# Optimization experiments

Measured on AMD Instinct MI355X. Metric: run time of the kernel, lower is better.

## Reference

```python
import jax, jax.numpy as jnp
import numpy as np

B, S, E = 2, 2048, 2048
H, HKV, D = 32, 8, 64  # n_heads, n_kv_heads, head_dim


def _rope(x, cos, sin):
    # x: [B,S,h,D]; cos/sin: [1,S,1,D//2]. Complex rotate on (even,odd) pairs.
    xp = x.reshape(*x.shape[:-1], D // 2, 2)
    x0, x1 = xp[..., 0], xp[..., 1]
    r0 = x0 * cos - x1 * sin
    r1 = x0 * sin + x1 * cos
    return jnp.stack([r0, r1], axis=-1).reshape(x.shape)


def setup_inputs() -> dict:
    key = jax.random.key(0)
    ks = jax.random.split(key, 8)
    sc = 0.02
    # real RoPE frequencies (theta=10000) for realism
    inv = 1.0 / (10000.0 ** (np.arange(0, D, 2, dtype=np.float32) / D))
    t = np.arange(S, dtype=np.float32)
    ang = np.outer(t, inv)  # [S, D/2]
    return {
        "x": jax.random.normal(ks[0], (B, S, E), jnp.float32),
        "start_pos": 0,
        "freqs_cos": jnp.asarray(np.cos(ang))[None, :, None, :],
        "freqs_sin": jnp.asarray(np.sin(ang))[None, :, None, :],
        "wq": jax.random.normal(ks[1], (E, H * D), jnp.float32) * sc,
        "wk": jax.random.normal(ks[2], (E, HKV * D), jnp.float32) * sc,
        "wv": jax.random.normal(ks[3], (E, HKV * D), jnp.float32) * sc,
        "out_w": jax.random.normal(ks[4], (H * D, E), jnp.float32) * sc,
        "out_b": jnp.zeros((E,), jnp.float32),
        "k_cache": jnp.zeros((B, S, HKV, D), jnp.float32),
        "v_cache": jnp.zeros((B, S, HKV, D), jnp.float32),
    }


def reference(x, start_pos, freqs_cos, freqs_sin, wq, wk, wv, out_w, out_b, k_cache, v_cache):
    b, s, _ = x.shape
    q = (x @ wq).reshape(b, s, H, D)
    k = (x @ wk).reshape(b, s, HKV, D)
    v = (x @ wv).reshape(b, s, HKV, D)
    q = _rope(q, freqs_cos[:, :s], freqs_sin[:, :s])
    k = _rope(k, freqs_cos[:, :s], freqs_sin[:, :s])
    # KV-cache append (torch code detaches before writing)
    k_cache = jax.lax.dynamic_update_slice(k_cache, jax.lax.stop_gradient(k), (0, start_pos, 0, 0))
    v_cache = jax.lax.dynamic_update_slice(v_cache, jax.lax.stop_gradient(v), (0, start_pos, 0, 0))
    keys = k_cache[:b, : start_pos + s]    # [b, T, HKV, D]
    values = v_cache[:b, : start_pos + s]
    g = H // HKV
    if g > 1:  # GQA head repeat
        keys = jnp.repeat(keys, g, axis=2)     # [b, T, H, D]
        values = jnp.repeat(values, g, axis=2)
    scores = jnp.einsum("bqhd,bkhd->bhqk", q, keys) / jnp.sqrt(jnp.float32(D))
    att = jax.nn.softmax(scores, axis=-1)  # NOTE: source applies no causal mask
    o = jnp.einsum("bhqk,bkhd->bqhd", att, values).reshape(b, s, H * D)
    return o @ out_w + out_b
```

## Files before the change

kernel.cpp:

```cpp
#include <hip/hip_runtime.h>
#include <math.h>

#define B_    2
#define S_    2048
#define E_    2048
#define H_    32
#define HKV_  8
#define D_    64

typedef __bf16 bf16x8 __attribute__((ext_vector_type(8)));
typedef float  f32x4  __attribute__((ext_vector_type(4)));
typedef float  f32x16 __attribute__((ext_vector_type(16)));
typedef unsigned int u32x2 __attribute__((ext_vector_type(2)));
typedef unsigned int u32x4 __attribute__((ext_vector_type(4)));

#define GPTR(x) ((const __attribute__((address_space(1))) void*)(x))
#define LPTR(x) ((__attribute__((address_space(3))) void*)(x))

#define QK_SCALE_LOG2E 0.18033688011112042f

__global__ __launch_bounds__(256) void convert_kernel(
    const float* __restrict__ in, __bf16* __restrict__ out, int n8)
{
    const int i = blockIdx.x * 256 + threadIdx.x;
    if (i >= n8) return;
    const float4 a = ((const float4*)in)[i * 2];
    const float4 b = ((const float4*)in)[i * 2 + 1];
    bf16x8 o;
    o[0] = (__bf16)a.x; o[1] = (__bf16)a.y; o[2] = (__bf16)a.z; o[3] = (__bf16)a.w;
    o[4] = (__bf16)b.x; o[5] = (__bf16)b.y; o[6] = (__bf16)b.z; o[7] = (__bf16)b.w;
    ((bf16x8*)out)[i] = o;
}

__global__ __launch_bounds__(256) void transpose_convert_all_kernel(
    const float* __restrict__ wq, const float* __restrict__ wk,
    const float* __restrict__ wv, const float* __restrict__ wo,
    __bf16* __restrict__ wT, __bf16* __restrict__ woT)
{
    const float* in; __bf16* out; int N, xb;
    const int x = blockIdx.x;
    if (x < 64)      { in = wq; out = wT;                        N = 2048; xb = x; }
    else if (x < 80) { in = wk; out = wT + (size_t)2048 * 2048;  N = 512;  xb = x - 64; }
    else if (x < 96) { in = wv; out = wT + (size_t)2560 * 2048;  N = 512;  xb = x - 80; }
    else             { in = wo; out = woT;                       N = 2048; xb = x - 96; }
    const int K = 2048;

    __shared__ float tile[32][33];
    const int k0 = blockIdx.y * 32, n0 = xb * 32;
    const int r  = threadIdx.x >> 3;
    const int c4 = (threadIdx.x & 7) * 4;
    const float4 v = *(const float4*)&in[(size_t)(k0 + r) * N + n0 + c4];
    tile[r][c4 + 0] = v.x; tile[r][c4 + 1] = v.y;
    tile[r][c4 + 2] = v.z; tile[r][c4 + 3] = v.w;
    __syncthreads();
    ushort4 o;
    __bf16 h0 = (__bf16)tile[c4 + 0][r]; o.x = __builtin_bit_cast(unsigned short, h0);
    __bf16 h1 = (__bf16)tile[c4 + 1][r]; o.y = __builtin_bit_cast(unsigned short, h1);
    __bf16 h2 = (__bf16)tile[c4 + 2][r]; o.z = __builtin_bit_cast(unsigned short, h2);
    __bf16 h3 = (__bf16)tile[c4 + 3][r]; o.w = __builtin_bit_cast(unsigned short, h3);
    *(ushort4*)&out[(size_t)(n0 + r) * K + k0 + c4] = o;
}

template<int BN> struct PG {
    static constexpr int BM     = 256;
    static constexpr int BK     = 32;
    static constexpr int ASLOT  = BM * BK;
    static constexpr int BSLOT  = BN * BK;
    static constexpr int SLOT   = ASLOT + BSLOT;
    static constexpr int BINSTR = BN / 128;
    static constexpr int L      = 2 + BINSTR;
    static constexpr int NJ     = BN / 64;
};

template<int BN>
__device__ __forceinline__ void stage_tile(
    const __bf16* __restrict__ A, const __bf16* __restrict__ Bt,
    int m0, int n0, int K, int T, __bf16* sl, int t, int wbase)
{
    using G = PG<BN>;
    const int k0   = T * G::BK;
    const int rsub = t >> 2;
    const int cp   = t & 3;
#pragma unroll
    for (int g = 0; g < 2; ++g) {
        const int row = g * 128 + rsub;
        const int cl  = cp ^ ((row >> 1) & 3);
        __builtin_amdgcn_global_load_lds(
            GPTR(A + (size_t)(m0 + row) * K + k0 + cl * 8),
            LPTR(sl + (g * 512 + wbase) * 8), 16, 0, 0);
    }
#pragma unroll
    for (int g = 0; g < G::BINSTR; ++g) {
        const int row = g * 128 + rsub;
        const int cl  = cp ^ ((row >> 1) & 3);
        __builtin_amdgcn_global_load_lds(
            GPTR(Bt + (size_t)(n0 + row) * K + k0 + cl * 8),
            LPTR(sl + G::ASLOT + (g * 512 + wbase) * 8), 16, 0, 0);
    }
}

template<int BN>
__device__ __forceinline__ void compute_tile(
    const __bf16* sl, int wrow, int wcol, int col, int quad,
    f32x4 acc[8][PG<BN>::NJ])
{
    using G = PG<BN>;
    bf16x8 af[8], bfr[G::NJ];
#pragma unroll
    for (int i = 0; i < 8; ++i) {
        const int m = wrow + i * 16 + col;
        af[i] = *(const bf16x8*)&sl[m * 32 + ((quad ^ ((m >> 1) & 3)) * 8)];
    }
#pragma unroll
    for (int j = 0; j < G::NJ; ++j) {
        const int n = wcol + j * 16 + col;
        bfr[j] = *(const bf16x8*)&sl[G::ASLOT + n * 32 + ((quad ^ ((n >> 1) & 3)) * 8)];
    }
    __builtin_amdgcn_s_setprio(1);
#pragma unroll
    for (int i = 0; i < 8; ++i)
#pragma unroll
        for (int j = 0; j < G::NJ; ++j)
            acc[i][j] = __builtin_amdgcn_mfma_f32_16x16x32_bf16(
                af[i], bfr[j], acc[i][j], 0, 0, 0);
    __builtin_amdgcn_s_setprio(0);
}

template<int BN>
__device__ __forceinline__ void gemm_pipe_body(
    const __bf16* __restrict__ A, const __bf16* __restrict__ Bt,
    int m0, int n0, int K, __bf16* sL, f32x4 acc[8][PG<BN>::NJ])
{
    using G = PG<BN>;
    const int t     = threadIdx.x;
    const int wbase = t & ~63;
    const int lane  = t & 63;
    const int col   = lane & 15;
    const int quad  = lane >> 4;
    const int w     = t >> 6;
    const int wrow  = (w >> 2) * 128;
    const int wcol  = (w & 3) * (BN / 4);
    const int NT    = K / G::BK;

    stage_tile<BN>(A, Bt, m0, n0, K, 0, sL + 0 * G::SLOT, t, wbase);
    stage_tile<BN>(A, Bt, m0, n0, K, 1, sL + 1 * G::SLOT, t, wbase);
    stage_tile<BN>(A, Bt, m0, n0, K, 2, sL + 2 * G::SLOT, t, wbase);

    int T = 0;
#pragma unroll 1
    for (; T < NT - 3; ++T) {
        asm volatile("s_waitcnt vmcnt(%0)" :: "n"(2 * G::L) : "memory");
        __builtin_amdgcn_s_barrier();
        stage_tile<BN>(A, Bt, m0, n0, K, T + 3, sL + ((T + 3) & 3) * G::SLOT, t, wbase);
        compute_tile<BN>(sL + (T & 3) * G::SLOT, wrow, wcol, col, quad, acc);
    }
    asm volatile("s_waitcnt vmcnt(%0)" :: "n"(2 * G::L) : "memory");
    __builtin_amdgcn_s_barrier();
    compute_tile<BN>(sL + (T & 3) * G::SLOT, wrow, wcol, col, quad, acc); ++T;
    asm volatile("s_waitcnt vmcnt(%0)" :: "n"(G::L) : "memory");
    __builtin_amdgcn_s_barrier();
    compute_tile<BN>(sL + (T & 3) * G::SLOT, wrow, wcol, col, quad, acc); ++T;
    asm volatile("s_waitcnt vmcnt(0)" ::: "memory");
    __builtin_amdgcn_s_barrier();
    compute_tile<BN>(sL + (T & 3) * G::SLOT, wrow, wcol, col, quad, acc);
}

__global__ __launch_bounds__(512, 2) void gemm_qkv_kernel(
    const __bf16* __restrict__ xb, const __bf16* __restrict__ wT,
    const float* __restrict__ fc, const float* __restrict__ fs,
    __bf16* __restrict__ qb, __bf16* __restrict__ kb, __bf16* __restrict__ vb)
{
    __shared__ __bf16 sL[4 * PG<256>::SLOT];
    f32x4 acc[8][4];
#pragma unroll
    for (int i = 0; i < 8; ++i)
#pragma unroll
        for (int j = 0; j < 4; ++j) acc[i][j] = (f32x4){0.f, 0.f, 0.f, 0.f};

    const int lin     = blockIdx.x;
    const int logical = (lin & 7) * 24 + (lin >> 3);
    const int bx      = logical % 12;
    const int m0      = (logical / 12) * 256;
    const int n0      = bx * 256;

    gemm_pipe_body<256>(xb, wT, m0, n0, E_, sL, acc);

    __bf16* Cp; int ldc, base;
    if (bx < 8)       { Cp = qb; ldc = H_ * D_;   base = 0;    }
    else if (bx < 10) { Cp = kb; ldc = HKV_ * D_; base = 2048; }
    else              { Cp = vb; ldc = HKV_ * D_; base = 2560; }
    const bool  doRope = (bx < 10);
    const float qsc    = (bx < 8) ? QK_SCALE_LOG2E : 1.0f;

    const int t    = threadIdx.x;
    const int lane = t & 63;
    const int col  = lane & 15;
    const int quad = lane >> 4;
    const int w    = t >> 6;
    const int wrow = (w >> 2) * 128;
    const int wcol = (w & 3) * 64;
#pragma unroll
    for (int i = 0; i < 8; ++i)
#pragma unroll
        for (int j = 0; j < 4; ++j)
#pragma unroll
            for (int r = 0; r < 4; ++r) {
                const int m  = m0 + wrow + i * 16 + quad * 4 + r;
                const int ng = n0 + wcol + j * 16 + col;
                float val = acc[i][j][r] * qsc;
                if (doRope) {
                    const int   s    = m & (S_ - 1);
                    const int   pair = (ng & 63) >> 1;
                    const float c    = fc[s * 32 + pair];
                    const float sn   = fs[s * 32 + pair];
                    const float oth  = __shfl_xor(val, 1);
                    val = (lane & 1) ? (oth * sn + val * c)
                                     : (val * c - oth * sn);
                }
                Cp[(size_t)m * ldc + (ng - base)] = (__bf16)val;
            }
}

__global__ __launch_bounds__(512, 2) void gemm_out_kernel(
    const __bf16* __restrict__ ob, const __bf16* __restrict__ woT,
    const float* __restrict__ bias, float* __restrict__ out)
{
    __shared__ __bf16 sL[4 * PG<128>::SLOT];
    f32x4 acc[8][2];
#pragma unroll
    for (int i = 0; i < 8; ++i)
#pragma unroll
        for (int j = 0; j < 2; ++j) acc[i][j] = (f32x4){0.f, 0.f, 0.f, 0.f};

    const int lin     = blockIdx.x;
    const int logical = (lin & 7) * 32 + (lin >> 3);
    const int n0      = (logical % 16) * 128;
    const int m0      = (logical / 16) * 256;

    gemm_pipe_body<128>(ob, woT, m0, n0, H_ * D_, sL, acc);

    const int t    = threadIdx.x;
    const int lane = t & 63;
    const int col  = lane & 15;
    const int quad = lane >> 4;
    const int w    = t >> 6;
    const int wrow = (w >> 2) * 128;
    const int wcol = (w & 3) * 32;
#pragma unroll
    for (int i = 0; i < 8; ++i)
#pragma unroll
        for (int j = 0; j < 2; ++j)
#pragma unroll
            for (int r = 0; r < 4; ++r) {
                const int m = m0 + wrow + i * 16 + quad * 4 + r;
                const int n = n0 + wcol + j * 16 + col;
                out[(size_t)m * E_ + n] = acc[i][j][r] + bias[n];
            }
}

struct StageRegs {
    bf16x8  k0, k1;
    ushort4 va0, vc0, va1, vc1;
};

__device__ __forceinline__ void stage_load(
    StageRegs& r, const __bf16* kbase, const __bf16* vbase, int j0,
    int kkey, int kd, int vkp, int vdg)
{
    const int KSTR = HKV_ * D_;
    const __bf16* kr = kbase + (size_t)(j0 + kkey) * KSTR + kd;
    r.k0 = ((const bf16x8*)kr)[0];
    r.k1 = ((const bf16x8*)kr)[1];
    const __bf16* v0 = vbase + (size_t)(j0 + vkp) * KSTR + vdg;
    r.va0 = *(const ushort4*)(v0);
    r.vc0 = *(const ushort4*)(v0 + KSTR);
    r.va1 = *(const ushort4*)(v0 + 32);
    r.vc1 = *(const ushort4*)(v0 + KSTR + 32);
}

__device__ __forceinline__ void stage_write(
    const StageRegs& r, __bf16 (*sK)[72], __bf16 (*sVT)[72],
    int kkey, int kd, int vkp, int vdg)
{
    *(bf16x8*)&sK[kkey][kd]     = r.k0;
    *(bf16x8*)&sK[kkey][kd + 8] = r.k1;
    *(unsigned int*)&sVT[vdg + 0][vkp]      = ((unsigned)r.vc0.x << 16) | r.va0.x;
    *(unsigned int*)&sVT[vdg + 1][vkp]      = ((unsigned)r.vc0.y << 16) | r.va0.y;
    *(unsigned int*)&sVT[vdg + 2][vkp]      = ((unsigned)r.vc0.z << 16) | r.va0.z;
    *(unsigned int*)&sVT[vdg + 3][vkp]      = ((unsigned)r.vc0.w << 16) | r.va0.w;
    *(unsigned int*)&sVT[vdg + 32 + 0][vkp] = ((unsigned)r.vc1.x << 16) | r.va1.x;
    *(unsigned int*)&sVT[vdg + 32 + 1][vkp] = ((unsigned)r.vc1.y << 16) | r.va1.y;
    *(unsigned int*)&sVT[vdg + 32 + 2][vkp] = ((unsigned)r.vc1.z << 16) | r.va1.z;
    *(unsigned int*)&sVT[vdg + 32 + 3][vkp] = ((unsigned)r.vc1.w << 16) | r.va1.w;
}

__device__ __forceinline__ bf16x8 pack_pa(const f32x16& p, int i0)
{
    unsigned a0, a1, a2, a3;
    asm("v_cvt_pk_bf16_f32 %0, %1, %2" : "=v"(a0) : "v"(p[i0 + 0]), "v"(p[i0 + 1]));
    asm("v_cvt_pk_bf16_f32 %0, %1, %2" : "=v"(a1) : "v"(p[i0 + 2]), "v"(p[i0 + 3]));
    asm("v_cvt_pk_bf16_f32 %0, %1, %2" : "=v"(a2) : "v"(p[i0 + 4]), "v"(p[i0 + 5]));
    asm("v_cvt_pk_bf16_f32 %0, %1, %2" : "=v"(a3) : "v"(p[i0 + 6]), "v"(p[i0 + 7]));
    const u32x2 s02 = __builtin_amdgcn_permlane32_swap(a0, a2, false, false);
    const u32x2 s13 = __builtin_amdgcn_permlane32_swap(a1, a3, false, false);
    return __builtin_bit_cast(bf16x8, (u32x4){s02[0], s13[0], s02[1], s13[1]});
}

__device__ __forceinline__ void attn_tile(
    const __bf16 (*sK)[72], const __bf16 (*sVT)[72],
    const bf16x8* bQ, int lq, int hi,
    f32x16& O0, f32x16& O1, float& lsum)
{
    f32x16 p0, p1;
#pragma unroll
    for (int i = 0; i < 16; ++i) { p0[i] = 0.f; p1[i] = 0.f; }
    __builtin_amdgcn_s_setprio(1);
#pragma unroll
    for (int ks = 0; ks < 4; ++ks) {
        const bf16x8 aK0 = *(const bf16x8*)&sK[lq][ks * 16 + hi * 8];
        const bf16x8 aK1 = *(const bf16x8*)&sK[32 + lq][ks * 16 + hi * 8];
        p0 = __builtin_amdgcn_mfma_f32_32x32x16_bf16(aK0, bQ[ks], p0, 0, 0, 0);
        p1 = __builtin_amdgcn_mfma_f32_32x32x16_bf16(aK1, bQ[ks], p1, 0, 0, 0);
    }
    __builtin_amdgcn_s_setprio(0);

    bf16x8 vbf[8];
#pragma unroll
    for (int ks = 0; ks < 4; ++ks) {
        vbf[ks * 2]     = *(const bf16x8*)&sVT[lq][ks * 16 + hi * 8];
        vbf[ks * 2 + 1] = *(const bf16x8*)&sVT[32 + lq][ks * 16 + hi * 8];
    }

    float ps = 0.f;
#pragma unroll
    for (int i = 0; i < 16; ++i) {
        p0[i] = __builtin_amdgcn_exp2f(p0[i]);
        p1[i] = __builtin_amdgcn_exp2f(p1[i]);
        ps += p0[i] + p1[i];
    }
    lsum += ps;

    bf16x8 pa[4];
    pa[0] = pack_pa(p0, 0);
    pa[1] = pack_pa(p0, 8);
    pa[2] = pack_pa(p1, 0);
    pa[3] = pack_pa(p1, 8);

    __builtin_amdgcn_s_setprio(1);
#pragma unroll
    for (int ks = 0; ks < 4; ++ks) {
        O0 = __builtin_amdgcn_mfma_f32_32x32x16_bf16(pa[ks], vbf[ks * 2],     O0, 0, 0, 0);
        O1 = __builtin_amdgcn_mfma_f32_32x32x16_bf16(pa[ks], vbf[ks * 2 + 1], O1, 0, 0, 0);
    }
    __builtin_amdgcn_s_setprio(0);
}

__global__ __launch_bounds__(256) void attn_kernel(
    const __bf16* __restrict__ qw, const __bf16* __restrict__ kw,
    const __bf16* __restrict__ vw, __bf16* __restrict__ ow)
{
    __shared__ __bf16 sK0[64][72], sVT0[64][72];
    __shared__ __bf16 sK1[64][72], sVT1[64][72];

    const int t    = threadIdx.x;
    const int lane = t & 63;
    const int w    = t >> 6;
    const int lq   = lane & 31;
    const int hi   = lane >> 5;

    const int bh  = blockIdx.y;
    const int b   = bh >> 5;
    const int h   = bh & 31;
    const int kvh = h >> 2;
    const int q0  = blockIdx.x * 128 + w * 32;

    bf16x8 bQ[4];
    {
        const __bf16* qrow = qw + (((size_t)b * S_ + q0 + lq) * H_ + h) * D_;
#pragma unroll
        for (int ks = 0; ks < 4; ++ks)
            bQ[ks] = *(const bf16x8*)(qrow + ks * 16 + hi * 8);
    }

    f32x16 O0, O1;
#pragma unroll
    for (int i = 0; i < 16; ++i) { O0[i] = 0.f; O1[i] = 0.f; }
    float lsum = 0.f;

    const __bf16* kbase = kw + ((size_t)b * S_ * HKV_ + kvh) * D_;
    const __bf16* vbase = vw + ((size_t)b * S_ * HKV_ + kvh) * D_;
    const int kkey = t >> 2,        kd  = (t & 3) * 16;
    const int vkp  = (t & 31) * 2,  vdg = (t >> 5) * 4;

    StageRegs sr;
    stage_load(sr, kbase, vbase, 0, kkey, kd, vkp, vdg);
    stage_write(sr, sK0, sVT0, kkey, kd, vkp, vdg);
    __syncthreads();

#pragma unroll 1
    for (int j0 = 0; j0 < S_; j0 += 128) {
        StageRegs nx;
        stage_load(nx, kbase, vbase, j0 + 64, kkey, kd, vkp, vdg);
        attn_tile(sK0, sVT0, bQ, lq, hi, O0, O1, lsum);
        stage_write(nx, sK1, sVT1, kkey, kd, vkp, vdg);
        __syncthreads();
        if (j0 + 128 < S_)
            stage_load(nx, kbase, vbase, j0 + 128, kkey, kd, vkp, vdg);
        attn_tile(sK1, sVT1, bQ, lq, hi, O0, O1, lsum);
        if (j0 + 128 < S_)
            stage_write(nx, sK0, sVT0, kkey, kd, vkp, vdg);
        __syncthreads();
    }

    lsum += __shfl_xor(lsum, 32);
    const float inv = 1.0f / lsum;

#pragma unroll
    for (int r = 0; r < 16; ++r) {
        const int   qr = (r & 3) + 8 * (r >> 2) + 4 * hi;
        const float li = __shfl(inv, qr);
        __bf16* orow = ow + (((size_t)b * S_ + q0 + qr) * H_ + h) * D_;
        orow[lq]      = (__bf16)(O0[r] * li);
        orow[32 + lq] = (__bf16)(O1[r] * li);
    }
}

extern "C" void kernel_launch(void* const* d_in, const int* in_sizes, int n_in,
                              void* d_out, int out_size, void* d_ws, size_t ws_size,
                              hipStream_t stream)
{
    const float* x  = (const float*)d_in[0];
    const float* fc = (const float*)d_in[2];
    const float* fs = (const float*)d_in[3];
    const float* wq = (const float*)d_in[4];
    const float* wk = (const float*)d_in[5];
    const float* wv = (const float*)d_in[6];
    const float* wo = (const float*)d_in[7];
    const float* obias = (const float*)d_in[8];
    float* out = (float*)d_out;

    __bf16* ws  = (__bf16*)d_ws;
    __bf16* xb  = ws;
    __bf16* wT  = xb  + (size_t)4096 * 2048;
    __bf16* woT = wT  + (size_t)3072 * 2048;
    __bf16* qb  = woT + (size_t)2048 * 2048;
    __bf16* kb  = qb  + (size_t)B_ * S_ * H_ * D_;
    __bf16* vb  = kb  + (size_t)B_ * S_ * HKV_ * D_;
    __bf16* obf = vb  + (size_t)B_ * S_ * HKV_ * D_;

    convert_kernel<<<4096, 256, 0, stream>>>(x, xb, 4096 * 2048 / 8);
    transpose_convert_all_kernel<<<dim3(160, 64), 256, 0, stream>>>(
        wq, wk, wv, wo, wT, woT);

    gemm_qkv_kernel<<<192, 512, 0, stream>>>(xb, wT, fc, fs, qb, kb, vb);

    attn_kernel<<<dim3(S_ / 128, B_ * H_), 256, 0, stream>>>(qb, kb, vb, obf);

    gemm_out_kernel<<<256, 512, 0, stream>>>(obf, woT, obias, out);
}
```

Baseline: 353.4 us.

## Process two 32-row query tiles per wave to reuse K/V shared-memory fragments

Each wave now handles 64 query rows (two 32-row sub-tiles) instead of 32. The K and V^T fragments are loaded from LDS once per 64-key tile and reused for both sub-tiles, which halves LDS reads and K/V global staging per query. The block now covers 256 query rows, so the grid is halved. In exchange, per-thread register use roughly doubles for the accumulators (launch bounds set to 256,2), which can lower occupancy, and the smaller grid (512 blocks) gives fewer blocks to spread across the CUs.

```diff
diff --git a/kernel.cpp b/kernel.cpp
--- a/kernel.cpp
+++ b/kernel.cpp
@@ -306,10 +306,8 @@
     return __builtin_bit_cast(bf16x8, (u32x4){s02[0], s13[0], s02[1], s13[1]});
 }
 
-__device__ __forceinline__ void attn_tile(
-    const __bf16 (*sK)[72], const __bf16 (*sVT)[72],
-    const bf16x8* bQ, int lq, int hi,
-    f32x16& O0, f32x16& O1, float& lsum)
+__device__ __forceinline__ void qk_sm_pack(
+    const bf16x8* aK, const bf16x8* bQ, bf16x8* pa, float& lsum)
 {
     f32x16 p0, p1;
 #pragma unroll
@@ -317,20 +315,10 @@
     __builtin_amdgcn_s_setprio(1);
 #pragma unroll
     for (int ks = 0; ks < 4; ++ks) {
-        const bf16x8 aK0 = *(const bf16x8*)&sK[lq][ks * 16 + hi * 8];
-        const bf16x8 aK1 = *(const bf16x8*)&sK[32 + lq][ks * 16 + hi * 8];
-        p0 = __builtin_amdgcn_mfma_f32_32x32x16_bf16(aK0, bQ[ks], p0, 0, 0, 0);
-        p1 = __builtin_amdgcn_mfma_f32_32x32x16_bf16(aK1, bQ[ks], p1, 0, 0, 0);
+        p0 = __builtin_amdgcn_mfma_f32_32x32x16_bf16(aK[ks * 2],     bQ[ks], p0, 0, 0, 0);
+        p1 = __builtin_amdgcn_mfma_f32_32x32x16_bf16(aK[ks * 2 + 1], bQ[ks], p1, 0, 0, 0);
     }
     __builtin_amdgcn_s_setprio(0);
-
-    bf16x8 vbf[8];
-#pragma unroll
-    for (int ks = 0; ks < 4; ++ks) {
-        vbf[ks * 2]     = *(const bf16x8*)&sVT[lq][ks * 16 + hi * 8];
-        vbf[ks * 2 + 1] = *(const bf16x8*)&sVT[32 + lq][ks * 16 + hi * 8];
-    }
-
     float ps = 0.f;
 #pragma unroll
     for (int i = 0; i < 16; ++i) {
@@ -339,23 +327,55 @@
         ps += p0[i] + p1[i];
     }
     lsum += ps;
-
-    bf16x8 pa[4];
     pa[0] = pack_pa(p0, 0);
     pa[1] = pack_pa(p0, 8);
     pa[2] = pack_pa(p1, 0);
     pa[3] = pack_pa(p1, 8);
+}
+
+__device__ __forceinline__ void attn_tile64(
+    const __bf16 (*sK)[72], const __bf16 (*sVT)[72],
+    const bf16x8* bQ0, const bf16x8* bQ1, int lq, int hi,
+    f32x16& O00, f32x16& O01, f32x16& O10, f32x16& O11,
+    float& ls0, float& ls1)
+{
+    bf16x8 aK[8];
+#pragma unroll
+    for (int ks = 0; ks < 4; ++ks) {
+        aK[ks * 2]     = *(const bf16x8*)&sK[lq][ks * 16 + hi * 8];
+        aK[ks * 2 + 1] = *(const bf16x8*)&sK[32 + lq][ks * 16 + hi * 8];
+    }
+
+    bf16x8 pa[4];
+    qk_sm_pack(aK, bQ0, pa, ls0);
+
+    bf16x8 vbf[8];
+#pragma unroll
+    for (int ks = 0; ks < 4; ++ks) {
+        vbf[ks * 2]     = *(const bf16x8*)&sVT[lq][ks * 16 + hi * 8];
+        vbf[ks * 2 + 1] = *(const bf16x8*)&sVT[32 + lq][ks * 16 + hi * 8];
+    }
 
     __builtin_amdgcn_s_setprio(1);
 #pragma unroll
     for (int ks = 0; ks < 4; ++ks) {
-        O0 = __builtin_amdgcn_mfma_f32_32x32x16_bf16(pa[ks], vbf[ks * 2],     O0, 0, 0, 0);
-        O1 = __builtin_amdgcn_mfma_f32_32x32x16_bf16(pa[ks], vbf[ks * 2 + 1], O1, 0, 0, 0);
+        O00 = __builtin_amdgcn_mfma_f32_32x32x16_bf16(pa[ks], vbf[ks * 2],     O00, 0, 0, 0);
+        O01 = __builtin_amdgcn_mfma_f32_32x32x16_bf16(pa[ks], vbf[ks * 2 + 1], O01, 0, 0, 0);
     }
     __builtin_amdgcn_s_setprio(0);
-}
-
-__global__ __launch_bounds__(256) void attn_kernel(
+
+    qk_sm_pack(aK, bQ1, pa, ls1);
+
+    __builtin_amdgcn_s_setprio(1);
+#pragma unroll
+    for (int ks = 0; ks < 4; ++ks) {
+        O10 = __builtin_amdgcn_mfma_f32_32x32x16_bf16(pa[ks], vbf[ks * 2],     O10, 0, 0, 0);
+        O11 = __builtin_amdgcn_mfma_f32_32x32x16_bf16(pa[ks], vbf[ks * 2 + 1], O11, 0, 0, 0);
+    }
+    __builtin_amdgcn_s_setprio(0);
+}
+
+__global__ __launch_bounds__(256, 2) void attn_kernel(
     const __bf16* __restrict__ qw, const __bf16* __restrict__ kw,
     const __bf16* __restrict__ vw, __bf16* __restrict__ ow)
 {
@@ -372,20 +392,23 @@
     const int b   = bh >> 5;
     const int h   = bh & 31;
     const int kvh = h >> 2;
-    const int q0  = blockIdx.x * 128 + w * 32;
-
-    bf16x8 bQ[4];
+    const int q0  = blockIdx.x * 256 + w * 64;
+
+    bf16x8 bQ0[4], bQ1[4];
     {
-        const __bf16* qrow = qw + (((size_t)b * S_ + q0 + lq) * H_ + h) * D_;
-#pragma unroll
-        for (int ks = 0; ks < 4; ++ks)
-            bQ[ks] = *(const bf16x8*)(qrow + ks * 16 + hi * 8);
-    }
-
-    f32x16 O0, O1;
-#pragma unroll
-    for (int i = 0; i < 16; ++i) { O0[i] = 0.f; O1[i] = 0.f; }
-    float lsum = 0.f;
+        const __bf16* qr0 = qw + (((size_t)b * S_ + q0 + lq) * H_ + h) * D_;
+        const __bf16* qr1 = qw + (((size_t)b * S_ + q0 + 32 + lq) * H_ + h) * D_;
+#pragma unroll
+        for (int ks = 0; ks < 4; ++ks) {
+            bQ0[ks] = *(const bf16x8*)(qr0 + ks * 16 + hi * 8);
+            bQ1[ks] = *(const bf16x8*)(qr1 + ks * 16 + hi * 8);
+        }
+    }
+
+    f32x16 O00, O01, O10, O11;
+#pragma unroll
+    for (int i = 0; i < 16; ++i) { O00[i] = 0.f; O01[i] = 0.f; O10[i] = 0.f; O11[i] = 0.f; }
+    float ls0 = 0.f, ls1 = 0.f;
 
     const __bf16* kbase = kw + ((size_t)b * S_ * HKV_ + kvh) * D_;
     const __bf16* vbase = vw + ((size_t)b * S_ * HKV_ + kvh) * D_;
@@ -401,27 +424,37 @@
     for (int j0 = 0; j0 < S_; j0 += 128) {
         StageRegs nx;
         stage_load(nx, kbase, vbase, j0 + 64, kkey, kd, vkp, vdg);
-        attn_tile(sK0, sVT0, bQ, lq, hi, O0, O1, lsum);
+        attn_tile64(sK0, sVT0, bQ0, bQ1, lq, hi, O00, O01, O10, O11, ls0, ls1);
         stage_write(nx, sK1, sVT1, kkey, kd, vkp, vdg);
         __syncthreads();
         if (j0 + 128 < S_)
             stage_load(nx, kbase, vbase, j0 + 128, kkey, kd, vkp, vdg);
-        attn_tile(sK1, sVT1, bQ, lq, hi, O0, O1, lsum);
+        attn_tile64(sK1, sVT1, bQ0, bQ1, lq, hi, O00, O01, O10, O11, ls0, ls1);
         if (j0 + 128 < S_)
             stage_write(nx, sK0, sVT0, kkey, kd, vkp, vdg);
         __syncthreads();
     }
 
-    lsum += __shfl_xor(lsum, 32);
-    const float inv = 1.0f / lsum;
+    ls0 += __shfl_xor(ls0, 32);
+    ls1 += __shfl_xor(ls1, 32);
+    const float inv0 = 1.0f / ls0;
+    const float inv1 = 1.0f / ls1;
 
 #pragma unroll
     for (int r = 0; r < 16; ++r) {
-        const int   qr = (r & 3) + 8 * (r >> 2) + 4 * hi;
-        const float li = __shfl(inv, qr);
-        __bf16* orow = ow + (((size_t)b * S_ + q0 + qr) * H_ + h) * D_;
-        orow[lq]      = (__bf16)(O0[r] * li);
-        orow[32 + lq] = (__bf16)(O1[r] * li);
+        const int qr = (r & 3) + 8 * (r >> 2) + 4 * hi;
+        {
+            const float li = __shfl(inv0, qr);
+            __bf16* orow = ow + (((size_t)b * S_ + q0 + qr) * H_ + h) * D_;
+            orow[lq]      = (__bf16)(O00[r] * li);
+            orow[32 + lq] = (__bf16)(O01[r] * li);
+        }
+        {
+            const float li = __shfl(inv1, qr);
+            __bf16* orow = ow + (((size_t)b * S_ + q0 + 32 + qr) * H_ + h) * D_;
+            orow[lq]      = (__bf16)(O10[r] * li);
+            orow[32 + lq] = (__bf16)(O11[r] * li);
+        }
     }
 }
 
@@ -454,7 +487,7 @@
 
     gemm_qkv_kernel<<<192, 512, 0, stream>>>(xb, wT, fc, fs, qb, kb, vb);
 
-    attn_kernel<<<dim3(S_ / 128, B_ * H_), 256, 0, stream>>>(qb, kb, vb, obf);
+    attn_kernel<<<dim3(S_ / 256, B_ * H_), 256, 0, stream>>>(qb, kb, vb, obf);
 
     gemm_out_kernel<<<256, 512, 0, stream>>>(obf, woT, obias, out);
 }
```

Result: slower. 447.4 us (+26.6%).

## Load K fragments directly from global, drop K LDS staging, remap grid for L2 locality

Applied to the files above, without the earlier changes.

The attention kernel no longer stages K tiles through shared memory. Each lane reads its MFMA K operand straight from global memory, which cuts LDS traffic and halves the shared allocation, and the kernel now declares 4 blocks per CU in its launch bounds. The 2D grid becomes a 1D grid of 1024 blocks remapped so that blocks sharing the same batch/KV head are grouped per XCD, so the four query heads of a KV group reuse K/V in L2. The cost is that K loads become uncoalesced, per-lane global loads sitting directly on the MFMA critical path with no prefetch, which adds latency exposure.

```diff
diff --git a/kernel.cpp b/kernel.cpp
--- a/kernel.cpp
+++ b/kernel.cpp
@@ -259,18 +259,13 @@
 }
 
 struct StageRegs {
-    bf16x8  k0, k1;
     ushort4 va0, vc0, va1, vc1;
 };
 
 __device__ __forceinline__ void stage_load(
-    StageRegs& r, const __bf16* kbase, const __bf16* vbase, int j0,
-    int kkey, int kd, int vkp, int vdg)
+    StageRegs& r, const __bf16* vbase, int j0, int vkp, int vdg)
 {
     const int KSTR = HKV_ * D_;
-    const __bf16* kr = kbase + (size_t)(j0 + kkey) * KSTR + kd;
-    r.k0 = ((const bf16x8*)kr)[0];
-    r.k1 = ((const bf16x8*)kr)[1];
     const __bf16* v0 = vbase + (size_t)(j0 + vkp) * KSTR + vdg;
     r.va0 = *(const ushort4*)(v0);
     r.vc0 = *(const ushort4*)(v0 + KSTR);
@@ -279,11 +274,8 @@
 }
 
 __device__ __forceinline__ void stage_write(
-    const StageRegs& r, __bf16 (*sK)[72], __bf16 (*sVT)[72],
-    int kkey, int kd, int vkp, int vdg)
-{
-    *(bf16x8*)&sK[kkey][kd]     = r.k0;
-    *(bf16x8*)&sK[kkey][kd + 8] = r.k1;
+    const StageRegs& r, __bf16 (*sVT)[72], int vkp, int vdg)
+{
     *(unsigned int*)&sVT[vdg + 0][vkp]      = ((unsigned)r.vc0.x << 16) | r.va0.x;
     *(unsigned int*)&sVT[vdg + 1][vkp]      = ((unsigned)r.vc0.y << 16) | r.va0.y;
     *(unsigned int*)&sVT[vdg + 2][vkp]      = ((unsigned)r.vc0.z << 16) | r.va0.z;
@@ -307,7 +299,7 @@
 }
 
 __device__ __forceinline__ void attn_tile(
-    const __bf16 (*sK)[72], const __bf16 (*sVT)[72],
+    const __bf16* kp0, const __bf16* kp1, const __bf16 (*sVT)[72],
     const bf16x8* bQ, int lq, int hi,
     f32x16& O0, f32x16& O1, float& lsum)
 {
@@ -317,8 +309,8 @@
     __builtin_amdgcn_s_setprio(1);
 #pragma unroll
     for (int ks = 0; ks < 4; ++ks) {
-        const bf16x8 aK0 = *(const bf16x8*)&sK[lq][ks * 16 + hi * 8];
-        const bf16x8 aK1 = *(const bf16x8*)&sK[32 + lq][ks * 16 + hi * 8];
+        const bf16x8 aK0 = *(const bf16x8*)(kp0 + ks * 16);
+        const bf16x8 aK1 = *(const bf16x8*)(kp1 + ks * 16);
         p0 = __builtin_amdgcn_mfma_f32_32x32x16_bf16(aK0, bQ[ks], p0, 0, 0, 0);
         p1 = __builtin_amdgcn_mfma_f32_32x32x16_bf16(aK1, bQ[ks], p1, 0, 0, 0);
     }
@@ -355,12 +347,11 @@
     __builtin_amdgcn_s_setprio(0);
 }
 
-__global__ __launch_bounds__(256) void attn_kernel(
+__global__ __launch_bounds__(256, 4) void attn_kernel(
     const __bf16* __restrict__ qw, const __bf16* __restrict__ kw,
     const __bf16* __restrict__ vw, __bf16* __restrict__ ow)
 {
-    __shared__ __bf16 sK0[64][72], sVT0[64][72];
-    __shared__ __bf16 sK1[64][72], sVT1[64][72];
+    __shared__ __bf16 sVT0[64][72], sVT1[64][72];
 
     const int t    = threadIdx.x;
     const int lane = t & 63;
@@ -368,11 +359,17 @@
     const int lq   = lane & 31;
     const int hi   = lane >> 5;
 
-    const int bh  = blockIdx.y;
-    const int b   = bh >> 5;
-    const int h   = bh & 31;
-    const int kvh = h >> 2;
-    const int q0  = blockIdx.x * 128 + w * 32;
+    const int wgid = blockIdx.x;
+    const int p    = wgid & 7;
+    const int idx  = wgid >> 3;
+    const int gkv  = p * 2 + (idx >> 6);
+    const int sub  = idx & 63;
+    const int hg   = sub >> 4;
+    const int qx   = sub & 15;
+    const int b    = gkv >> 3;
+    const int kvh  = gkv & 7;
+    const int h    = kvh * 4 + hg;
+    const int q0   = qx * 128 + w * 32;
 
     bf16x8 bQ[4];
     {
@@ -387,28 +384,33 @@
     for (int i = 0; i < 16; ++i) { O0[i] = 0.f; O1[i] = 0.f; }
     float lsum = 0.f;
 
+    const int KSTR = HKV_ * D_;
     const __bf16* kbase = kw + ((size_t)b * S_ * HKV_ + kvh) * D_;
     const __bf16* vbase = vw + ((size_t)b * S_ * HKV_ + kvh) * D_;
-    const int kkey = t >> 2,        kd  = (t & 3) * 16;
-    const int vkp  = (t & 31) * 2,  vdg = (t >> 5) * 4;
+    const __bf16* krow0 = kbase + (size_t)lq * KSTR + hi * 8;
+    const __bf16* krow1 = krow0 + (size_t)32 * KSTR;
+
+    const int vkp = (t & 31) * 2, vdg = (t >> 5) * 4;
 
     StageRegs sr;
-    stage_load(sr, kbase, vbase, 0, kkey, kd, vkp, vdg);
-    stage_write(sr, sK0, sVT0, kkey, kd, vkp, vdg);
+    stage_load(sr, vbase, 0, vkp, vdg);
+    stage_write(sr, sVT0, vkp, vdg);
     __syncthreads();
 
 #pragma unroll 1
     for (int j0 = 0; j0 < S_; j0 += 128) {
         StageRegs nx;
-        stage_load(nx, kbase, vbase, j0 + 64, kkey, kd, vkp, vdg);
-        attn_tile(sK0, sVT0, bQ, lq, hi, O0, O1, lsum);
-        stage_write(nx, sK1, sVT1, kkey, kd, vkp, vdg);
+        stage_load(nx, vbase, j0 + 64, vkp, vdg);
+        attn_tile(krow0 + (size_t)j0 * KSTR, krow1 + (size_t)j0 * KSTR,
+                  sVT0, bQ, lq, hi, O0, O1, lsum);
+        stage_write(nx, sVT1, vkp, vdg);
         __syncthreads();
         if (j0 + 128 < S_)
-            stage_load(nx, kbase, vbase, j0 + 128, kkey, kd, vkp, vdg);
-        attn_tile(sK1, sVT1, bQ, lq, hi, O0, O1, lsum);
+            stage_load(nx, vbase, j0 + 128, vkp, vdg);
+        attn_tile(krow0 + (size_t)(j0 + 64) * KSTR, krow1 + (size_t)(j0 + 64) * KSTR,
+                  sVT1, bQ, lq, hi, O0, O1, lsum);
         if (j0 + 128 < S_)
-            stage_write(nx, sK0, sVT0, kkey, kd, vkp, vdg);
+            stage_write(nx, sVT0, vkp, vdg);
         __syncthreads();
     }
 
@@ -454,7 +456,7 @@
 
     gemm_qkv_kernel<<<192, 512, 0, stream>>>(xb, wT, fc, fs, qb, kb, vb);
 
-    attn_kernel<<<dim3(S_ / 128, B_ * H_), 256, 0, stream>>>(qb, kb, vb, obf);
+    attn_kernel<<<1024, 256, 0, stream>>>(qb, kb, vb, obf);
 
     gemm_out_kernel<<<256, 512, 0, stream>>>(obf, woT, obias, out);
 }
```

Result: slower. 618.8 us (+75.1%).

## Replace GEMM pipeline with 8-phase half-tile ping-pong schedule and 256x256 out tiles

Applied to the files above, without the earlier changes.

Rewrites the shared GEMM mainloop to use BK=64 half-tiles (128x64) in two LDS buffers. Each K-step is split into eight phases that interleave fragment reads, async global-to-LDS loads of the next half-tile and MFMA quadrants, with a barrier around every phase, to overlap memory traffic with matrix work more finely. The output projection now uses 256x256 tiles with 128 blocks instead of 256x128 with 256 blocks. This raises per-block reuse but lowers parallelism on the CU count and adds many barriers.

```diff
diff --git a/kernel.cpp b/kernel.cpp
--- a/kernel.cpp
+++ b/kernel.cpp
@@ -61,108 +61,139 @@
     *(ushort4*)&out[(size_t)(n0 + r) * K + k0 + c4] = o;
 }
 
-template<int BN> struct PG {
-    static constexpr int BM     = 256;
-    static constexpr int BK     = 32;
-    static constexpr int ASLOT  = BM * BK;
-    static constexpr int BSLOT  = BN * BK;
-    static constexpr int SLOT   = ASLOT + BSLOT;
-    static constexpr int BINSTR = BN / 128;
-    static constexpr int L      = 2 + BINSTR;
-    static constexpr int NJ     = BN / 64;
-};
-
-template<int BN>
-__device__ __forceinline__ void stage_tile(
+#define SWZ(row, col) ((row) * 64 + ((col) ^ (((row) & 4) << 2)))
+
+__device__ __forceinline__ __bf16* ht_ptr(__bf16* sL, int c, int mat, int half)
+{
+    return sL + (((c * 2 + mat) * 2 + half) * (128 * 64));
+}
+
+__device__ __forceinline__ void stage_ht(
+    const __bf16* __restrict__ src, int ld, int row0, int k0,
+    __bf16* dst, int t)
+{
+#pragma unroll
+    for (int g = 0; g < 2; ++g) {
+        const int row = g * 64 + (t >> 3);
+        const int ch  = (t & 7) ^ ((row & 4) >> 1);
+        __builtin_amdgcn_global_load_lds(
+            GPTR(src + (size_t)(row0 + row) * ld + k0 + ch * 8),
+            LPTR(dst + row * 64 + (t & 7) * 8), 16, 0, 0);
+    }
+}
+
+__device__ __forceinline__ void read_a(
+    const __bf16* aht, int mh, int col16, int quad, bf16x8 fr[4][2])
+{
+#pragma unroll
+    for (int i = 0; i < 4; ++i) {
+        const int r = mh * 64 + i * 16 + col16;
+#pragma unroll
+        for (int ks = 0; ks < 2; ++ks)
+            fr[i][ks] = *(const bf16x8*)&aht[SWZ(r, ks * 32 + quad * 8)];
+    }
+}
+
+__device__ __forceinline__ void read_b(
+    const __bf16* bht, int bofs, int nh, int col16, int quad, bf16x8 fr[2][2])
+{
+#pragma unroll
+    for (int j = 0; j < 2; ++j) {
+        const int r = bofs + (nh * 2 + j) * 16 + col16;
+#pragma unroll
+        for (int ks = 0; ks < 2; ++ks)
+            fr[j][ks] = *(const bf16x8*)&bht[SWZ(r, ks * 32 + quad * 8)];
+    }
+}
+
+__device__ __forceinline__ void mfma_quad(
+    const bf16x8 a[4][2], const bf16x8 b[2][2], f32x4 acc[8][4], int mh, int nh)
+{
+    __builtin_amdgcn_s_setprio(1);
+#pragma unroll
+    for (int i = 0; i < 4; ++i)
+#pragma unroll
+        for (int j = 0; j < 2; ++j)
+#pragma unroll
+            for (int ks = 0; ks < 2; ++ks)
+                acc[mh * 4 + i][nh * 2 + j] = __builtin_amdgcn_mfma_f32_16x16x32_bf16(
+                    a[i][ks], b[j][ks], acc[mh * 4 + i][nh * 2 + j], 0, 0, 0);
+    __builtin_amdgcn_s_setprio(0);
+}
+
+#define MIDBAR() do { __builtin_amdgcn_s_barrier(); \
+    asm volatile("s_waitcnt lgkmcnt(0)" ::: "memory"); \
+    __builtin_amdgcn_sched_barrier(0); } while (0)
+#define ENDBAR() __builtin_amdgcn_s_barrier()
+
+__device__ __forceinline__ void gemm8_body(
     const __bf16* __restrict__ A, const __bf16* __restrict__ Bt,
-    int m0, int n0, int K, int T, __bf16* sl, int t, int wbase)
-{
-    using G = PG<BN>;
-    const int k0   = T * G::BK;
-    const int rsub = t >> 2;
-    const int cp   = t & 3;
-#pragma unroll
-    for (int g = 0; g < 2; ++g) {
-        const int row = g * 128 + rsub;
-        const int cl  = cp ^ ((row >> 1) & 3);
-        __builtin_amdgcn_global_load_lds(
-            GPTR(A + (size_t)(m0 + row) * K + k0 + cl * 8),
-            LPTR(sl + (g * 512 + wbase) * 8), 16, 0, 0);
-    }
-#pragma unroll
-    for (int g = 0; g < G::BINSTR; ++g) {
-        const int row = g * 128 + rsub;
-        const int cl  = cp ^ ((row >> 1) & 3);
-        __builtin_amdgcn_global_load_lds(
-            GPTR(Bt + (size_t)(n0 + row) * K + k0 + cl * 8),
-            LPTR(sl + G::ASLOT + (g * 512 + wbase) * 8), 16, 0, 0);
-    }
-}
-
-template<int BN>
-__device__ __forceinline__ void compute_tile(
-    const __bf16* sl, int wrow, int wcol, int col, int quad,
-    f32x4 acc[8][PG<BN>::NJ])
-{
-    using G = PG<BN>;
-    bf16x8 af[8], bfr[G::NJ];
-#pragma unroll
-    for (int i = 0; i < 8; ++i) {
-        const int m = wrow + i * 16 + col;
-        af[i] = *(const bf16x8*)&sl[m * 32 + ((quad ^ ((m >> 1) & 3)) * 8)];
-    }
-#pragma unroll
-    for (int j = 0; j < G::NJ; ++j) {
-        const int n = wcol + j * 16 + col;
-        bfr[j] = *(const bf16x8*)&sl[G::ASLOT + n * 32 + ((quad ^ ((n >> 1) & 3)) * 8)];
-    }
-    __builtin_amdgcn_s_setprio(1);
-#pragma unroll
-    for (int i = 0; i < 8; ++i)
-#pragma unroll
-        for (int j = 0; j < G::NJ; ++j)
-            acc[i][j] = __builtin_amdgcn_mfma_f32_16x16x32_bf16(
-                af[i], bfr[j], acc[i][j], 0, 0, 0);
-    __builtin_amdgcn_s_setprio(0);
-}
-
-template<int BN>
-__device__ __forceinline__ void gemm_pipe_body(
-    const __bf16* __restrict__ A, const __bf16* __restrict__ Bt,
-    int m0, int n0, int K, __bf16* sL, f32x4 acc[8][PG<BN>::NJ])
-{
-    using G = PG<BN>;
+    int m0, int n0, int K, __bf16* sL, f32x4 acc[8][4])
+{
     const int t     = threadIdx.x;
-    const int wbase = t & ~63;
     const int lane  = t & 63;
-    const int col   = lane & 15;
+    const int w     = t >> 6;
+    const int col16 = lane & 15;
     const int quad  = lane >> 4;
-    const int w     = t >> 6;
-    const int wrow  = (w >> 2) * 128;
-    const int wcol  = (w & 3) * (BN / 4);
-    const int NT    = K / G::BK;
-
-    stage_tile<BN>(A, Bt, m0, n0, K, 0, sL + 0 * G::SLOT, t, wbase);
-    stage_tile<BN>(A, Bt, m0, n0, K, 1, sL + 1 * G::SLOT, t, wbase);
-    stage_tile<BN>(A, Bt, m0, n0, K, 2, sL + 2 * G::SLOT, t, wbase);
-
-    int T = 0;
+    const int wr    = w >> 2;
+    const int wc    = w & 3;
+    const int NT    = K / 64;
+
+    stage_ht(A,  K, m0 + 0,   0,  ht_ptr(sL, 0, 0, 0), t);
+    stage_ht(A,  K, m0 + 128, 0,  ht_ptr(sL, 0, 0, 1), t);
+    stage_ht(Bt, K, n0 + 0,   0,  ht_ptr(sL, 0, 1, 0), t);
+    stage_ht(Bt, K, n0 + 128, 0,  ht_ptr(sL, 0, 1, 1), t);
+    stage_ht(A,  K, m0 + 0,   64, ht_ptr(sL, 1, 0, 0), t);
+    stage_ht(A,  K, m0 + 128, 64, ht_ptr(sL, 1, 0, 1), t);
+    asm volatile("s_waitcnt vmcnt(4)" ::: "memory");
+    __builtin_amdgcn_s_barrier();
+
+    const __bf16* myA[2] = { ht_ptr(sL, 0, 0, wr),      ht_ptr(sL, 1, 0, wr) };
+    const __bf16* myB[2] = { ht_ptr(sL, 0, 1, wc >> 1), ht_ptr(sL, 1, 1, wc >> 1) };
+    const int bofs = (wc & 1) * 64;
+
+    bf16x8 a0[4][2], a1[4][2], b0f[2][2], b1f[2][2];
+
 #pragma unroll 1
-    for (; T < NT - 3; ++T) {
-        asm volatile("s_waitcnt vmcnt(%0)" :: "n"(2 * G::L) : "memory");
-        __builtin_amdgcn_s_barrier();
-        stage_tile<BN>(A, Bt, m0, n0, K, T + 3, sL + ((T + 3) & 3) * G::SLOT, t, wbase);
-        compute_tile<BN>(sL + (T & 3) * G::SLOT, wrow, wcol, col, quad, acc);
-    }
-    asm volatile("s_waitcnt vmcnt(%0)" :: "n"(2 * G::L) : "memory");
-    __builtin_amdgcn_s_barrier();
-    compute_tile<BN>(sL + (T & 3) * G::SLOT, wrow, wcol, col, quad, acc); ++T;
-    asm volatile("s_waitcnt vmcnt(%0)" :: "n"(G::L) : "memory");
-    __builtin_amdgcn_s_barrier();
-    compute_tile<BN>(sL + (T & 3) * G::SLOT, wrow, wcol, col, quad, acc); ++T;
-    asm volatile("s_waitcnt vmcnt(0)" ::: "memory");
-    __builtin_amdgcn_s_barrier();
-    compute_tile<BN>(sL + (T & 3) * G::SLOT, wrow, wcol, col, quad, acc);
+    for (int I = 0; I < NT / 2; ++I) {
+        const int k1  = (2 * I + 1) * 64;
+        const int kt2 = (2 * I + 2 < NT) ? 2 * I + 2 : NT - 1;
+        const int kt3 = (2 * I + 3 < NT) ? 2 * I + 3 : NT - 1;
+
+        read_a(myA[0], 0, col16, quad, a0);
+        read_b(myB[0], bofs, 0, col16, quad, b0f);
+        stage_ht(Bt, K, n0 + 0, k1, ht_ptr(sL, 1, 1, 0), t);
+        MIDBAR(); mfma_quad(a0, b0f, acc, 0, 0); ENDBAR();
+
+        read_a(myA[0], 1, col16, quad, a1);
+        stage_ht(Bt, K, n0 + 128, k1, ht_ptr(sL, 1, 1, 1), t);
+        MIDBAR(); mfma_quad(a1, b0f, acc, 1, 0); ENDBAR();
+
+        read_b(myB[0], bofs, 1, col16, quad, b1f);
+        stage_ht(A, K, m0 + 0, kt2 * 64, ht_ptr(sL, 0, 0, 0), t);
+        MIDBAR(); mfma_quad(a1, b1f, acc, 1, 1); ENDBAR();
+
+        stage_ht(A, K, m0 + 128, kt2 * 64, ht_ptr(sL, 0, 0, 1), t);
+        asm volatile("s_waitcnt vmcnt(4)" ::: "memory");
+        MIDBAR(); mfma_quad(a0, b1f, acc, 0, 1); ENDBAR();
+
+        read_a(myA[1], 0, col16, quad, a0);
+        read_b(myB[1], bofs, 0, col16, quad, b0f);
+        stage_ht(Bt, K, n0 + 0, kt2 * 64, ht_ptr(sL, 0, 1, 0), t);
+        MIDBAR(); mfma_quad(a0, b0f, acc, 0, 0); ENDBAR();
+
+        read_a(myA[1], 1, col16, quad, a1);
+        stage_ht(Bt, K, n0 + 128, kt2 * 64, ht_ptr(sL, 0, 1, 1), t);
+        MIDBAR(); mfma_quad(a1, b0f, acc, 1, 0); ENDBAR();
+
+        read_b(myB[1], bofs, 1, col16, quad, b1f);
+        stage_ht(A, K, m0 + 0, kt3 * 64, ht_ptr(sL, 1, 0, 0), t);
+        MIDBAR(); mfma_quad(a1, b1f, acc, 1, 1); ENDBAR();
+
+        stage_ht(A, K, m0 + 128, kt3 * 64, ht_ptr(sL, 1, 0, 1), t);
+        asm volatile("s_waitcnt vmcnt(4)" ::: "memory");
+        MIDBAR(); mfma_quad(a0, b1f, acc, 0, 1); ENDBAR();
+    }
 }
 
 __global__ __launch_bounds__(512, 2) void gemm_qkv_kernel(
@@ -170,7 +201,7 @@
     const float* __restrict__ fc, const float* __restrict__ fs,
     __bf16* __restrict__ qb, __bf16* __restrict__ kb, __bf16* __restrict__ vb)
 {
-    __shared__ __bf16 sL[4 * PG<256>::SLOT];
+    __shared__ __bf16 sL[8 * 128 * 64];
     f32x4 acc[8][4];
 #pragma unroll
     for (int i = 0; i < 8; ++i)
@@ -183,7 +214,7 @@
     const int m0      = (logical / 12) * 256;
     const int n0      = bx * 256;
 
-    gemm_pipe_body<256>(xb, wT, m0, n0, E_, sL, acc);
+    gemm8_body(xb, wT, m0, n0, E_, sL, acc);
 
     __bf16* Cp; int ldc, base;
     if (bx < 8)       { Cp = qb; ldc = H_ * D_;   base = 0;    }
@@ -192,13 +223,13 @@
     const bool  doRope = (bx < 10);
     const float qsc    = (bx < 8) ? QK_SCALE_LOG2E : 1.0f;
 
-    const int t    = threadIdx.x;
-    const int lane = t & 63;
-    const int col  = lane & 15;
-    const int quad = lane >> 4;
-    const int w    = t >> 6;
-    const int wrow = (w >> 2) * 128;
-    const int wcol = (w & 3) * 64;
+    const int t     = threadIdx.x;
+    const int lane  = t & 63;
+    const int col16 = lane & 15;
+    const int quad  = lane >> 4;
+    const int w     = t >> 6;
+    const int wrow  = (w >> 2) * 128;
+    const int wcol  = (w & 3) * 64;
 #pragma unroll
     for (int i = 0; i < 8; ++i)
 #pragma unroll
@@ -206,7 +237,7 @@
 #pragma unroll
             for (int r = 0; r < 4; ++r) {
                 const int m  = m0 + wrow + i * 16 + quad * 4 + r;
-                const int ng = n0 + wcol + j * 16 + col;
+                const int ng = n0 + wcol + j * 16 + col16;
                 float val = acc[i][j][r] * qsc;
                 if (doRope) {
                     const int   s    = m & (S_ - 1);
@@ -225,35 +256,35 @@
     const __bf16* __restrict__ ob, const __bf16* __restrict__ woT,
     const float* __restrict__ bias, float* __restrict__ out)
 {
-    __shared__ __bf16 sL[4 * PG<128>::SLOT];
-    f32x4 acc[8][2];
+    __shared__ __bf16 sL[8 * 128 * 64];
+    f32x4 acc[8][4];
 #pragma unroll
     for (int i = 0; i < 8; ++i)
 #pragma unroll
-        for (int j = 0; j < 2; ++j) acc[i][j] = (f32x4){0.f, 0.f, 0.f, 0.f};
+        for (int j = 0; j < 4; ++j) acc[i][j] = (f32x4){0.f, 0.f, 0.f, 0.f};
 
     const int lin     = blockIdx.x;
-    const int logical = (lin & 7) * 32 + (lin >> 3);
-    const int n0      = (logical % 16) * 128;
-    const int m0      = (logical / 16) * 256;
-
-    gemm_pipe_body<128>(ob, woT, m0, n0, H_ * D_, sL, acc);
-
-    const int t    = threadIdx.x;
-    const int lane = t & 63;
-    const int col  = lane & 15;
-    const int quad = lane >> 4;
-    const int w    = t >> 6;
-    const int wrow = (w >> 2) * 128;
-    const int wcol = (w & 3) * 32;
+    const int logical = (lin & 7) * 16 + (lin >> 3);
+    const int n0      = (logical % 8) * 256;
+    const int m0      = (logical / 8) * 256;
+
+    gemm8_body(ob, woT, m0, n0, H_ * D_, sL, acc);
+
+    const int t     = threadIdx.x;
+    const int lane  = t & 63;
+    const int col16 = lane & 15;
+    const int quad  = lane >> 4;
+    const int w     = t >> 6;
+    const int wrow  = (w >> 2) * 128;
+    const int wcol  = (w & 3) * 64;
 #pragma unroll
     for (int i = 0; i < 8; ++i)
 #pragma unroll
-        for (int j = 0; j < 2; ++j)
+        for (int j = 0; j < 4; ++j)
 #pragma unroll
             for (int r = 0; r < 4; ++r) {
                 const int m = m0 + wrow + i * 16 + quad * 4 + r;
-                const int n = n0 + wcol + j * 16 + col;
+                const int n = n0 + wcol + j * 16 + col16;
                 out[(size_t)m * E_ + n] = acc[i][j][r] + bias[n];
             }
 }
@@ -456,5 +487,5 @@
 
     attn_kernel<<<dim3(S_ / 128, B_ * H_), 256, 0, stream>>>(qb, kb, vb, obf);
 
-    gemm_out_kernel<<<256, 512, 0, stream>>>(obf, woT, obias, out);
-}
+    gemm_out_kernel<<<128, 512, 0, stream>>>(obf, woT, obias, out);
+}
```

Result: slower. 482.1 us (+36.4%).
